# Optimization experiments

Measured on AMD Instinct MI355X. Metric: run time of the kernel, lower is better.

The kernel has to match this reference:

```python
import jax, jax.numpy as jnp
import numpy as np

EPS_RMS = 1e-6
EPS_Q = 1e-5
EPS_NORM = 1e-10


def _rmsnorm(x):
    return x * jax.lax.rsqrt(jnp.mean(x * x, axis=-1, keepdims=True) + EPS_RMS)


def _activation_quant(x):
    # per-token 8-bit absmax quantization (BitNet b1.58)
    scale = 127.0 / jnp.maximum(jnp.max(jnp.abs(x), axis=-1, keepdims=True), EPS_Q)
    return jnp.clip(jnp.round(x * scale), -128.0, 127.0) / scale


def _weight_quant(w):
    # per-tensor ternary quantization with mean-abs scale
    scale = 1.0 / jnp.maximum(jnp.mean(jnp.abs(w)), EPS_Q)
    return jnp.clip(jnp.round(w * scale), -1.0, 1.0) / scale


def _bitlinear(x, w, b):
    xn = _rmsnorm(x)
    xq = xn + jax.lax.stop_gradient(_activation_quant(xn) - xn)  # STE
    wq = w + jax.lax.stop_gradient(_weight_quant(w) - w)         # STE
    return jnp.einsum('bsf,of->bso', xq, wq) + b


def setup_inputs() -> dict:
    key = jax.random.key(0)
    ks = jax.random.split(key, 4)
    B, S, F = 32, 1024, 512
    evidence_features = jax.random.normal(ks[0], (B, S, F), dtype=jnp.float32)
    prior_belief = jax.random.uniform(ks[1], (B, S, F), dtype=jnp.float32)
    W1 = jax.random.normal(ks[2], (F, 2 * F), dtype=jnp.float32) * (1.0 / np.sqrt(2 * F))
    b1 = jnp.zeros((F,), dtype=jnp.float32)
    W2 = jax.random.normal(ks[3], (F, F), dtype=jnp.float32) * (1.0 / np.sqrt(F))
    b2 = jnp.zeros((F,), dtype=jnp.float32)
    return {"evidence_features": evidence_features, "prior_belief": prior_belief,
            "W1": W1, "b1": b1, "W2": W2, "b2": b2}


def reference(evidence_features, prior_belief, W1, b1, W2, b2):
    # belief_update MLP on concat(prior, evidence)
    update_input = jnp.concatenate([prior_belief, evidence_features], axis=-1)  # [B,S,2F]
    h = jax.nn.relu(_bitlinear(update_input, W1, b1))                           # [B,S,F]
    likelihood_factors = jax.nn.sigmoid(_bitlinear(h, W2, b2))                  # [B,S,F]
    posterior_unnorm = prior_belief * likelihood_factors
    normalizer = jnp.maximum(jnp.sum(posterior_unnorm, axis=1, keepdims=True), EPS_NORM)
    return posterior_unnorm / normalizer
```

## Files before the change

kernel.cpp:

```cpp
#include <hip/hip_runtime.h>
#include <math.h>

typedef __attribute__((ext_vector_type(4))) int i32x4;
typedef __attribute__((ext_vector_type(4))) float f32x4;

#define GLOAD_LDS16(g, l)                                          \
  __builtin_amdgcn_global_load_lds(                                \
      (const __attribute__((address_space(1))) void*)(g),          \
      (__attribute__((address_space(3))) void*)(l), 16, 0, 0)

__global__ void kWabs(const float* __restrict__ w1, const float* __restrict__ w2,
                      double* __restrict__ part) {
  const bool second = blockIdx.x >= 256;
  const float* w = second ? w2 : w1;
  const int n = second ? 262144 : 524288;
  int t = (blockIdx.x & 255) * 256 + threadIdx.x;
  double s = 0.0;
  for (int i = t; i < n; i += 65536) s += (double)fabsf(w[i]);
#pragma unroll
  for (int m = 32; m >= 1; m >>= 1) s += __shfl_xor(s, m);
  __shared__ double sd[4];
  int lane = threadIdx.x & 63, wid = threadIdx.x >> 6;
  if (lane == 0) sd[wid] = s;
  __syncthreads();
  if (threadIdx.x == 0) part[blockIdx.x] = (sd[0] + sd[1]) + (sd[2] + sd[3]);
}

__global__ void kWfin(const double* __restrict__ part, float* __restrict__ wsv) {
  const double* p = part + blockIdx.x * 256;
  const double n = (blockIdx.x == 0) ? 524288.0 : 262144.0;
  double s = p[threadIdx.x];
#pragma unroll
  for (int m = 32; m >= 1; m >>= 1) s += __shfl_xor(s, m);
  __shared__ double sd[4];
  int lane = threadIdx.x & 63, wid = threadIdx.x >> 6;
  if (lane == 0) sd[wid] = s;
  __syncthreads();
  if (threadIdx.x == 0) {
    double tot = (sd[0] + sd[1]) + (sd[2] + sd[3]);
    wsv[blockIdx.x] = fmaxf((float)(tot / n), 1e-5f);
  }
}

__global__ void kWq(const float* __restrict__ w1, const float* __restrict__ w2,
                    const float* __restrict__ wsv,
                    char* __restrict__ wq1, char* __restrict__ wq2) {
  const bool second = blockIdx.x >= 2048;
  const float* w = second ? w2 : w1;
  char* wq = second ? wq2 : wq1;
  const float scale = 1.0f / wsv[second ? 1 : 0];
  int i = (second ? blockIdx.x - 2048 : blockIdx.x) * 256 + threadIdx.x;
  float q = fminf(fmaxf(rintf(w[i] * scale), -1.0f), 1.0f);
  wq[i] = (char)(int)q;
}

__global__ __launch_bounds__(512, 4) void kFused1(
    const float* __restrict__ prior, const float* __restrict__ evid,
    const char* __restrict__ Wq, const float* __restrict__ biasG,
    const float* __restrict__ wS,
    char* __restrict__ XqOut, float* __restrict__ rActOut) {
  __shared__ __align__(16) union {
    char Ap[65536];
    struct { float sq[64][8]; float mx[64][8]; } ep;
  } u;
  __shared__ float rowSc[64];
  __shared__ float biasS[512];

  const int tid = threadIdx.x;
  const int lane = tid & 63;
  const int wn = tid >> 6;
  const int lr = lane & 15;
  const int kg = lane >> 4;
  const size_t row0 = (size_t)blockIdx.x * 64;

  biasS[tid] = biasG[tid];

  {
    const int lc = lane * 4;
    const float* pp = prior + (row0 + wn * 8) * 512 + lc;
    const float* pe = evid + (row0 + wn * 8) * 512 + lc;
    f32x4 x0 = *(const f32x4*)pp;
    f32x4 x1 = *(const f32x4*)(pp + 256);
    f32x4 x2 = *(const f32x4*)pe;
    f32x4 x3 = *(const f32x4*)(pe + 256);
#pragma unroll
    for (int rr = 0; rr < 8; ++rr) {
      f32x4 y0, y1, y2, y3;
      if (rr < 7) {
        const float* np = pp + (rr + 1) * 512;
        const float* ne = pe + (rr + 1) * 512;
        y0 = *(const f32x4*)np; y1 = *(const f32x4*)(np + 256);
        y2 = *(const f32x4*)ne; y3 = *(const f32x4*)(ne + 256);
      }
      float ss = 0.f, mx = 0.f;
      f32x4 xs[4] = {x0, x1, x2, x3};
#pragma unroll
      for (int v = 0; v < 4; ++v)
#pragma unroll
        for (int i = 0; i < 4; ++i) { float f = xs[v][i]; ss += f * f; mx = fmaxf(mx, fabsf(f)); }
#pragma unroll
      for (int m = 32; m >= 1; m >>= 1) { ss += __shfl_xor(ss, m); mx = fmaxf(mx, __shfl_xor(mx, m)); }
      const float inv = 1.0f / sqrtf(ss * (1.0f / 1024.0f) + 1e-6f);
      const float amax = fmaxf(mx * inv, 1e-5f);
      const float s = 127.0f / amax;
      int pk[4];
#pragma unroll
      for (int v = 0; v < 4; ++v) {
        int p = 0;
#pragma unroll
        for (int i = 0; i < 4; ++i) {
          int qi = (int)fminf(fmaxf(rintf(xs[v][i] * inv * s), -128.0f), 127.0f);
          p |= (qi & 255) << (8 * i);
        }
        pk[v] = p;
      }
      const int r = wn * 8 + rr;
      const int base = r * 1024 + (lc ^ ((r & 7) << 4));
      *(int*)&u.Ap[base] = pk[0];
      *(int*)&u.Ap[base + 256] = pk[1];
      *(int*)&u.Ap[base + 512] = pk[2];
      *(int*)&u.Ap[base + 768] = pk[3];
      if (lane == 0) rowSc[r] = amax / 127.0f;
      if (rr < 7) { x0 = y0; x1 = y1; x2 = y2; x3 = y3; }
    }
  }

  i32x4 acc[4][4];
#pragma unroll
  for (int a = 0; a < 4; ++a)
#pragma unroll
    for (int b = 0; b < 4; ++b) acc[a][b] = (i32x4){0, 0, 0, 0};

  const char* gBl = Wq + (size_t)(wn * 64 + lr) * 1024 + kg * 16;
  i32x4 bf[4];
#pragma unroll
  for (int fn = 0; fn < 4; ++fn)
    bf[fn] = *(const i32x4*)(gBl + fn * 16384);

  __syncthreads();

  const int aswz = (lr & 7) << 4;
#pragma unroll 2
  for (int kt = 0; kt < 16; ++kt) {
    i32x4 bn[4];
    if (kt < 15) {
#pragma unroll
      for (int fn = 0; fn < 4; ++fn)
        bn[fn] = *(const i32x4*)(gBl + (kt + 1) * 64 + fn * 16384);
    }
    const int acol = (kt * 64 + kg * 16) ^ aswz;
    i32x4 af[4];
#pragma unroll
    for (int fm = 0; fm < 4; ++fm)
      af[fm] = *(const i32x4*)&u.Ap[(fm * 16 + lr) * 1024 + acol];
#pragma unroll
    for (int fn = 0; fn < 4; ++fn)
#pragma unroll
      for (int fm = 0; fm < 4; ++fm)
        acc[fm][fn] = __builtin_amdgcn_mfma_i32_16x16x64_i8(af[fm], bf[fn], acc[fm][fn], 0, 0, 0);
#pragma unroll
    for (int fn = 0; fn < 4; ++fn) bf[fn] = bn[fn];
  }

  __syncthreads();

  const float wsv_ = wS[0];
  f32x4 fa[4][4];
#pragma unroll
  for (int fm = 0; fm < 4; ++fm) {
    float sc[4];
#pragma unroll
    for (int j = 0; j < 4; ++j) sc[j] = rowSc[fm * 16 + kg * 4 + j] * wsv_;
#pragma unroll
    for (int fn = 0; fn < 4; ++fn) {
      const float bb = biasS[wn * 64 + fn * 16 + lr];
#pragma unroll
      for (int j = 0; j < 4; ++j)
        fa[fm][fn][j] = fmaxf((float)acc[fm][fn][j] * sc[j] + bb, 0.0f);
    }
  }
#pragma unroll
  for (int fm = 0; fm < 4; ++fm)
#pragma unroll
    for (int j = 0; j < 4; ++j) {
      float ss = 0.f, mx = 0.f;
#pragma unroll
      for (int fn = 0; fn < 4; ++fn) { float h = fa[fm][fn][j]; ss += h * h; mx = fmaxf(mx, h); }
#pragma unroll
      for (int m = 8; m >= 1; m >>= 1) { ss += __shfl_xor(ss, m); mx = fmaxf(mx, __shfl_xor(mx, m)); }
      if (lr == 0) {
        int rl = fm * 16 + kg * 4 + j;
        u.ep.sq[rl][wn] = ss;
        u.ep.mx[rl][wn] = mx;
      }
    }
  __syncthreads();
#pragma unroll
  for (int fm = 0; fm < 4; ++fm)
#pragma unroll
    for (int j = 0; j < 4; ++j) {
      const int rl = fm * 16 + kg * 4 + j;
      float sst = 0.f, mxt = 0.f;
#pragma unroll
      for (int w = 0; w < 8; ++w) {
        sst += u.ep.sq[rl][w];
        mxt = fmaxf(mxt, u.ep.mx[rl][w]);
      }
      float inv = 1.0f / sqrtf(sst * (1.0f / 512.0f) + 1e-6f);
      float amax = fmaxf(mxt * inv, 1e-5f);
      float s = 127.0f / amax;
      if (lr == 0 && wn == 0) rActOut[row0 + rl] = amax / 127.0f;
#pragma unroll
      for (int fn = 0; fn < 4; ++fn) {
        float xn = fa[fm][fn][j] * inv;
        int qi = (int)fminf(fmaxf(rintf(xn * s), -128.0f), 127.0f);
        XqOut[(row0 + rl) * 512 + wn * 64 + fn * 16 + lr] = (char)qi;
      }
    }
}

__global__ __launch_bounds__(512, 4) void kGemm2(
    const char* __restrict__ Xq, const char* __restrict__ Wq,
    const float* __restrict__ biasG, const float* __restrict__ rAct,
    const float* __restrict__ wS, const float* __restrict__ prior,
    float* __restrict__ outUn, float* __restrict__ partG) {
  __shared__ __align__(16) char A[32768];
  __shared__ float rowR[64];
  __shared__ float biasS[512];
  __shared__ float normPart[512];

  const int tid = threadIdx.x;
  const int lane = tid & 63;
  const int wn = tid >> 6;
  const int lr = lane & 15;
  const int kg = lane >> 4;
  const size_t row0 = (size_t)blockIdx.x * 64;

  if (tid < 64) rowR[tid] = rAct[row0 + tid];
  biasS[tid] = biasG[tid];

#pragma unroll
  for (int i = 0; i < 4; ++i) {
    const int r = i * 16 + wn * 2 + (lane >> 5);
    const int cs = ((lane & 31) * 16) ^ ((r & 7) << 4);
    GLOAD_LDS16(Xq + (row0 + r) * 512 + cs, &A[i * 8192 + wn * 1024]);
  }

  const char* gBl = Wq + (size_t)(wn * 64 + lr) * 512 + kg * 16;
  i32x4 bf[4];
#pragma unroll
  for (int fn = 0; fn < 4; ++fn)
    bf[fn] = *(const i32x4*)(gBl + fn * 8192);

  i32x4 acc[4][4];
#pragma unroll
  for (int a = 0; a < 4; ++a)
#pragma unroll
    for (int b = 0; b < 4; ++b) acc[a][b] = (i32x4){0, 0, 0, 0};

  __syncthreads();

  const int aswz = (lr & 7) << 4;
#pragma unroll 2
  for (int kt = 0; kt < 8; ++kt) {
    i32x4 bn[4];
    if (kt < 7) {
#pragma unroll
      for (int fn = 0; fn < 4; ++fn)
        bn[fn] = *(const i32x4*)(gBl + (kt + 1) * 64 + fn * 8192);
    }
    const int acol = (kt * 64 + kg * 16) ^ aswz;
    i32x4 af[4];
#pragma unroll
    for (int fm = 0; fm < 4; ++fm)
      af[fm] = *(const i32x4*)&A[(fm * 16 + lr) * 512 + acol];
#pragma unroll
    for (int fn = 0; fn < 4; ++fn)
#pragma unroll
      for (int fm = 0; fm < 4; ++fm)
        acc[fm][fn] = __builtin_amdgcn_mfma_i32_16x16x64_i8(af[fm], bf[fn], acc[fm][fn], 0, 0, 0);
#pragma unroll
    for (int fn = 0; fn < 4; ++fn) bf[fn] = bn[fn];
  }

  const float wsv_ = wS[0];
  float colsum[4] = {0.f, 0.f, 0.f, 0.f};
#pragma unroll
  for (int fm = 0; fm < 4; ++fm) {
    float sc[4];
#pragma unroll
    for (int j = 0; j < 4; ++j) sc[j] = rowR[fm * 16 + kg * 4 + j] * wsv_;
#pragma unroll
    for (int fn = 0; fn < 4; ++fn) {
      const int col = wn * 64 + fn * 16 + lr;
      const float bb = biasS[col];
#pragma unroll
      for (int j = 0; j < 4; ++j) {
        const size_t rg = row0 + fm * 16 + kg * 4 + j;
        float v = (float)acc[fm][fn][j] * sc[j] + bb;
        float like = 1.0f / (1.0f + expf(-v));
        float un = prior[rg * 512 + col] * like;
        outUn[rg * 512 + col] = un;
        colsum[fn] += un;
      }
    }
  }
#pragma unroll
  for (int fn = 0; fn < 4; ++fn) {
    colsum[fn] += __shfl_xor(colsum[fn], 16);
    colsum[fn] += __shfl_xor(colsum[fn], 32);
  }
  if (lane < 16) {
#pragma unroll
    for (int fn = 0; fn < 4; ++fn) normPart[wn * 64 + fn * 16 + lane] = colsum[fn];
  }
  __syncthreads();
  partG[(size_t)blockIdx.x * 512 + tid] = normPart[tid];
}

__global__ void kNorm1(const float* __restrict__ partG, float* __restrict__ normA) {
  const int b = blockIdx.x, f = threadIdx.x;
  float s = 0.f;
#pragma unroll
  for (int i = 0; i < 16; ++i) s += partG[(size_t)(b * 16 + i) * 512 + f];
  normA[b * 512 + f] = fmaxf(s, 1e-10f);
}

__global__ void kNorm2(float* __restrict__ out, const float* __restrict__ normA) {
  const size_t i4 = (size_t)blockIdx.x * blockDim.x + threadIdx.x;
  f32x4 v = ((const f32x4*)out)[i4];
  const int f4 = (int)(i4 & 127);
  const int b = (int)(i4 >> 17);
  f32x4 n = ((const f32x4*)normA)[b * 128 + f4];
  v[0] /= n[0]; v[1] /= n[1]; v[2] /= n[2]; v[3] /= n[3];
  ((f32x4*)out)[i4] = v;
}

extern "C" void kernel_launch(void* const* d_in, const int* in_sizes, int n_in,
                              void* d_out, int out_size, void* d_ws, size_t ws_size,
                              hipStream_t stream) {
  const float* evid  = (const float*)d_in[0];
  const float* prior = (const float*)d_in[1];
  const float* W1    = (const float*)d_in[2];
  const float* b1    = (const float*)d_in[3];
  const float* W2    = (const float*)d_in[4];
  const float* b2    = (const float*)d_in[5];
  float* out = (float*)d_out;

  char* ws = (char*)d_ws;
  char*   X2q   = ws;
  char*   W1q   = ws + 16777216;
  char*   W2q   = ws + 17301504;
  float*  r2    = (float*)(ws + 17563648);
  double* part  = (double*)(ws + 17694720);
  float*  wsv   = (float*)(ws + 17698816);
  float*  partG = (float*)(ws + 17699072);
  float*  normA = (float*)(ws + 18747648);

  kWabs<<<512, 256, 0, stream>>>(W1, W2, part);
  kWfin<<<2, 256, 0, stream>>>(part, wsv);
  kWq<<<3072, 256, 0, stream>>>(W1, W2, wsv, W1q, W2q);
  kFused1<<<512, 512, 0, stream>>>(prior, evid, W1q, b1, wsv + 0, X2q, r2);
  kGemm2<<<512, 512, 0, stream>>>(X2q, W2q, b2, r2, wsv + 1, prior, out, partG);
  kNorm1<<<32, 512, 0, stream>>>(partG, normA);
  kNorm2<<<16384, 256, 0, stream>>>(out, normA);
}
```

Baseline: 135.6 us.

## Recompute GEMM2 twice to fuse normalization and drop unnormalized output round-trip

Removes the kNorm1/kNorm2 kernels. GEMM2 now runs twice: the first pass only produces per-block column sums, and the second pass reduces those partials itself and writes the normalized output directly. This avoids writing the 64MB unnormalized tensor and then reading and writing it again, at the cost of repeating the int8 GEMM, sigmoid and prior read. It also double-buffers B-fragment prefetch two steps ahead with full unroll in both GEMMs, and processes rows in pairs during kFused1's quantization prologue to gain more memory-level parallelism.

```diff
diff --git a/kernel.cpp b/kernel.cpp
--- a/kernel.cpp
+++ b/kernel.cpp
@@ -79,49 +79,71 @@
     const int lc = lane * 4;
     const float* pp = prior + (row0 + wn * 8) * 512 + lc;
     const float* pe = evid + (row0 + wn * 8) * 512 + lc;
-    f32x4 x0 = *(const f32x4*)pp;
-    f32x4 x1 = *(const f32x4*)(pp + 256);
-    f32x4 x2 = *(const f32x4*)pe;
-    f32x4 x3 = *(const f32x4*)(pe + 256);
-#pragma unroll
-    for (int rr = 0; rr < 8; ++rr) {
-      f32x4 y0, y1, y2, y3;
-      if (rr < 7) {
-        const float* np = pp + (rr + 1) * 512;
-        const float* ne = pe + (rr + 1) * 512;
-        y0 = *(const f32x4*)np; y1 = *(const f32x4*)(np + 256);
-        y2 = *(const f32x4*)ne; y3 = *(const f32x4*)(ne + 256);
-      }
-      float ss = 0.f, mx = 0.f;
-      f32x4 xs[4] = {x0, x1, x2, x3};
-#pragma unroll
-      for (int v = 0; v < 4; ++v)
-#pragma unroll
-        for (int i = 0; i < 4; ++i) { float f = xs[v][i]; ss += f * f; mx = fmaxf(mx, fabsf(f)); }
-#pragma unroll
-      for (int m = 32; m >= 1; m >>= 1) { ss += __shfl_xor(ss, m); mx = fmaxf(mx, __shfl_xor(mx, m)); }
-      const float inv = 1.0f / sqrtf(ss * (1.0f / 1024.0f) + 1e-6f);
-      const float amax = fmaxf(mx * inv, 1e-5f);
-      const float s = 127.0f / amax;
-      int pk[4];
-#pragma unroll
-      for (int v = 0; v < 4; ++v) {
-        int p = 0;
-#pragma unroll
-        for (int i = 0; i < 4; ++i) {
-          int qi = (int)fminf(fmaxf(rintf(xs[v][i] * inv * s), -128.0f), 127.0f);
-          p |= (qi & 255) << (8 * i);
+    f32x4 x[2][4];
+#pragma unroll
+    for (int r = 0; r < 2; ++r) {
+      x[r][0] = *(const f32x4*)(pp + r * 512);
+      x[r][1] = *(const f32x4*)(pp + r * 512 + 256);
+      x[r][2] = *(const f32x4*)(pe + r * 512);
+      x[r][3] = *(const f32x4*)(pe + r * 512 + 256);
+    }
+#pragma unroll
+    for (int pr = 0; pr < 4; ++pr) {
+      f32x4 y[2][4];
+      if (pr < 3) {
+#pragma unroll
+        for (int r = 0; r < 2; ++r) {
+          const float* np = pp + (pr * 2 + 2 + r) * 512;
+          const float* ne = pe + (pr * 2 + 2 + r) * 512;
+          y[r][0] = *(const f32x4*)np; y[r][1] = *(const f32x4*)(np + 256);
+          y[r][2] = *(const f32x4*)ne; y[r][3] = *(const f32x4*)(ne + 256);
         }
-        pk[v] = p;
-      }
-      const int r = wn * 8 + rr;
-      const int base = r * 1024 + (lc ^ ((r & 7) << 4));
-      *(int*)&u.Ap[base] = pk[0];
-      *(int*)&u.Ap[base + 256] = pk[1];
-      *(int*)&u.Ap[base + 512] = pk[2];
-      *(int*)&u.Ap[base + 768] = pk[3];
-      if (lane == 0) rowSc[r] = amax / 127.0f;
-      if (rr < 7) { x0 = y0; x1 = y1; x2 = y2; x3 = y3; }
+      }
+      float ss[2] = {0.f, 0.f}, mx[2] = {0.f, 0.f};
+#pragma unroll
+      for (int r = 0; r < 2; ++r)
+#pragma unroll
+        for (int v = 0; v < 4; ++v)
+#pragma unroll
+          for (int i = 0; i < 4; ++i) {
+            float f = x[r][v][i];
+            ss[r] += f * f; mx[r] = fmaxf(mx[r], fabsf(f));
+          }
+#pragma unroll
+      for (int m = 32; m >= 1; m >>= 1) {
+        ss[0] += __shfl_xor(ss[0], m); ss[1] += __shfl_xor(ss[1], m);
+        mx[0] = fmaxf(mx[0], __shfl_xor(mx[0], m)); mx[1] = fmaxf(mx[1], __shfl_xor(mx[1], m));
+      }
+#pragma unroll
+      for (int r = 0; r < 2; ++r) {
+        const float inv = 1.0f / sqrtf(ss[r] * (1.0f / 1024.0f) + 1e-6f);
+        const float amax = fmaxf(mx[r] * inv, 1e-5f);
+        const float s = 127.0f / amax;
+        int pk[4];
+#pragma unroll
+        for (int v = 0; v < 4; ++v) {
+          int p = 0;
+#pragma unroll
+          for (int i = 0; i < 4; ++i) {
+            int qi = (int)fminf(fmaxf(rintf(x[r][v][i] * inv * s), -128.0f), 127.0f);
+            p |= (qi & 255) << (8 * i);
+          }
+          pk[v] = p;
+        }
+        const int rw = wn * 8 + pr * 2 + r;
+        const int base = rw * 1024 + (lc ^ ((rw & 7) << 4));
+        *(int*)&u.Ap[base] = pk[0];
+        *(int*)&u.Ap[base + 256] = pk[1];
+        *(int*)&u.Ap[base + 512] = pk[2];
+        *(int*)&u.Ap[base + 768] = pk[3];
+        if (lane == 0) rowSc[rw] = amax / 127.0f;
+      }
+      if (pr < 3) {
+#pragma unroll
+        for (int r = 0; r < 2; ++r)
+#pragma unroll
+          for (int v = 0; v < 4; ++v) x[r][v] = y[r][v];
+      }
     }
   }
 
@@ -132,22 +154,19 @@
     for (int b = 0; b < 4; ++b) acc[a][b] = (i32x4){0, 0, 0, 0};
 
   const char* gBl = Wq + (size_t)(wn * 64 + lr) * 1024 + kg * 16;
-  i32x4 bf[4];
-#pragma unroll
-  for (int fn = 0; fn < 4; ++fn)
-    bf[fn] = *(const i32x4*)(gBl + fn * 16384);
+  i32x4 bf0[4], bf1[4];
+#pragma unroll
+  for (int fn = 0; fn < 4; ++fn) {
+    bf0[fn] = *(const i32x4*)(gBl + fn * 16384);
+    bf1[fn] = *(const i32x4*)(gBl + 64 + fn * 16384);
+  }
 
   __syncthreads();
 
   const int aswz = (lr & 7) << 4;
-#pragma unroll 2
+#pragma unroll
   for (int kt = 0; kt < 16; ++kt) {
-    i32x4 bn[4];
-    if (kt < 15) {
-#pragma unroll
-      for (int fn = 0; fn < 4; ++fn)
-        bn[fn] = *(const i32x4*)(gBl + (kt + 1) * 64 + fn * 16384);
-    }
+    i32x4(&bfc)[4] = (kt & 1) ? bf1 : bf0;
     const int acol = (kt * 64 + kg * 16) ^ aswz;
     i32x4 af[4];
 #pragma unroll
@@ -157,9 +176,12 @@
     for (int fn = 0; fn < 4; ++fn)
 #pragma unroll
       for (int fm = 0; fm < 4; ++fm)
-        acc[fm][fn] = __builtin_amdgcn_mfma_i32_16x16x64_i8(af[fm], bf[fn], acc[fm][fn], 0, 0, 0);
-#pragma unroll
-    for (int fn = 0; fn < 4; ++fn) bf[fn] = bn[fn];
+        acc[fm][fn] = __builtin_amdgcn_mfma_i32_16x16x64_i8(af[fm], bfc[fn], acc[fm][fn], 0, 0, 0);
+    if (kt + 2 < 16) {
+#pragma unroll
+      for (int fn = 0; fn < 4; ++fn)
+        bfc[fn] = *(const i32x4*)(gBl + (kt + 2) * 64 + fn * 16384);
+    }
   }
 
   __syncthreads();
@@ -219,15 +241,16 @@
     }
 }
 
+template <bool WRITE_PASS>
 __global__ __launch_bounds__(512, 4) void kGemm2(
     const char* __restrict__ Xq, const char* __restrict__ Wq,
     const float* __restrict__ biasG, const float* __restrict__ rAct,
     const float* __restrict__ wS, const float* __restrict__ prior,
-    float* __restrict__ outUn, float* __restrict__ partG) {
+    float* __restrict__ outp, float* __restrict__ partG) {
   __shared__ __align__(16) char A[32768];
   __shared__ float rowR[64];
   __shared__ float biasS[512];
-  __shared__ float normPart[512];
+  __shared__ float normS[512];
 
   const int tid = threadIdx.x;
   const int lane = tid & 63;
@@ -246,11 +269,21 @@
     GLOAD_LDS16(Xq + (row0 + r) * 512 + cs, &A[i * 8192 + wn * 1024]);
   }
 
+  if constexpr (WRITE_PASS) {
+    const int b = blockIdx.x >> 4;
+    float ns = 0.f;
+#pragma unroll
+    for (int i = 0; i < 16; ++i) ns += partG[(size_t)(b * 16 + i) * 512 + tid];
+    normS[tid] = fmaxf(ns, 1e-10f);
+  }
+
   const char* gBl = Wq + (size_t)(wn * 64 + lr) * 512 + kg * 16;
-  i32x4 bf[4];
-#pragma unroll
-  for (int fn = 0; fn < 4; ++fn)
-    bf[fn] = *(const i32x4*)(gBl + fn * 8192);
+  i32x4 bf0[4], bf1[4];
+#pragma unroll
+  for (int fn = 0; fn < 4; ++fn) {
+    bf0[fn] = *(const i32x4*)(gBl + fn * 8192);
+    bf1[fn] = *(const i32x4*)(gBl + 64 + fn * 8192);
+  }
 
   i32x4 acc[4][4];
 #pragma unroll
@@ -261,14 +294,9 @@
   __syncthreads();
 
   const int aswz = (lr & 7) << 4;
-#pragma unroll 2
+#pragma unroll
   for (int kt = 0; kt < 8; ++kt) {
-    i32x4 bn[4];
-    if (kt < 7) {
-#pragma unroll
-      for (int fn = 0; fn < 4; ++fn)
-        bn[fn] = *(const i32x4*)(gBl + (kt + 1) * 64 + fn * 8192);
-    }
+    i32x4(&bfc)[4] = (kt & 1) ? bf1 : bf0;
     const int acol = (kt * 64 + kg * 16) ^ aswz;
     i32x4 af[4];
 #pragma unroll
@@ -278,62 +306,69 @@
     for (int fn = 0; fn < 4; ++fn)
 #pragma unroll
       for (int fm = 0; fm < 4; ++fm)
-        acc[fm][fn] = __builtin_amdgcn_mfma_i32_16x16x64_i8(af[fm], bf[fn], acc[fm][fn], 0, 0, 0);
-#pragma unroll
-    for (int fn = 0; fn < 4; ++fn) bf[fn] = bn[fn];
+        acc[fm][fn] = __builtin_amdgcn_mfma_i32_16x16x64_i8(af[fm], bfc[fn], acc[fm][fn], 0, 0, 0);
+    if (kt + 2 < 8) {
+#pragma unroll
+      for (int fn = 0; fn < 4; ++fn)
+        bfc[fn] = *(const i32x4*)(gBl + (kt + 2) * 64 + fn * 8192);
+    }
   }
 
   const float wsv_ = wS[0];
-  float colsum[4] = {0.f, 0.f, 0.f, 0.f};
-#pragma unroll
-  for (int fm = 0; fm < 4; ++fm) {
-    float sc[4];
-#pragma unroll
-    for (int j = 0; j < 4; ++j) sc[j] = rowR[fm * 16 + kg * 4 + j] * wsv_;
+  if constexpr (!WRITE_PASS) {
+    float colsum[4] = {0.f, 0.f, 0.f, 0.f};
+#pragma unroll
+    for (int fm = 0; fm < 4; ++fm) {
+      float sc[4];
+#pragma unroll
+      for (int j = 0; j < 4; ++j) sc[j] = rowR[fm * 16 + kg * 4 + j] * wsv_;
+#pragma unroll
+      for (int fn = 0; fn < 4; ++fn) {
+        const int col = wn * 64 + fn * 16 + lr;
+        const float bb = biasS[col];
+#pragma unroll
+        for (int j = 0; j < 4; ++j) {
+          const size_t rg = row0 + fm * 16 + kg * 4 + j;
+          float v = (float)acc[fm][fn][j] * sc[j] + bb;
+          float like = 1.0f / (1.0f + expf(-v));
+          float un = prior[rg * 512 + col] * like;
+          colsum[fn] += un;
+        }
+      }
+    }
 #pragma unroll
     for (int fn = 0; fn < 4; ++fn) {
-      const int col = wn * 64 + fn * 16 + lr;
-      const float bb = biasS[col];
-#pragma unroll
-      for (int j = 0; j < 4; ++j) {
-        const size_t rg = row0 + fm * 16 + kg * 4 + j;
-        float v = (float)acc[fm][fn][j] * sc[j] + bb;
-        float like = 1.0f / (1.0f + expf(-v));
-        float un = prior[rg * 512 + col] * like;
-        outUn[rg * 512 + col] = un;
-        colsum[fn] += un;
-      }
-    }
-  }
-#pragma unroll
-  for (int fn = 0; fn < 4; ++fn) {
-    colsum[fn] += __shfl_xor(colsum[fn], 16);
-    colsum[fn] += __shfl_xor(colsum[fn], 32);
-  }
-  if (lane < 16) {
-#pragma unroll
-    for (int fn = 0; fn < 4; ++fn) normPart[wn * 64 + fn * 16 + lane] = colsum[fn];
-  }
-  __syncthreads();
-  partG[(size_t)blockIdx.x * 512 + tid] = normPart[tid];
-}
-
-__global__ void kNorm1(const float* __restrict__ partG, float* __restrict__ normA) {
-  const int b = blockIdx.x, f = threadIdx.x;
-  float s = 0.f;
-#pragma unroll
-  for (int i = 0; i < 16; ++i) s += partG[(size_t)(b * 16 + i) * 512 + f];
-  normA[b * 512 + f] = fmaxf(s, 1e-10f);
-}
-
-__global__ void kNorm2(float* __restrict__ out, const float* __restrict__ normA) {
-  const size_t i4 = (size_t)blockIdx.x * blockDim.x + threadIdx.x;
-  f32x4 v = ((const f32x4*)out)[i4];
-  const int f4 = (int)(i4 & 127);
-  const int b = (int)(i4 >> 17);
-  f32x4 n = ((const f32x4*)normA)[b * 128 + f4];
-  v[0] /= n[0]; v[1] /= n[1]; v[2] /= n[2]; v[3] /= n[3];
-  ((f32x4*)out)[i4] = v;
+      colsum[fn] += __shfl_xor(colsum[fn], 16);
+      colsum[fn] += __shfl_xor(colsum[fn], 32);
+    }
+    if (lane < 16) {
+#pragma unroll
+      for (int fn = 0; fn < 4; ++fn) normS[wn * 64 + fn * 16 + lane] = colsum[fn];
+    }
+    __syncthreads();
+    partG[(size_t)blockIdx.x * 512 + tid] = normS[tid];
+  } else {
+#pragma unroll
+    for (int fm = 0; fm < 4; ++fm) {
+      float sc[4];
+#pragma unroll
+      for (int j = 0; j < 4; ++j) sc[j] = rowR[fm * 16 + kg * 4 + j] * wsv_;
+#pragma unroll
+      for (int fn = 0; fn < 4; ++fn) {
+        const int col = wn * 64 + fn * 16 + lr;
+        const float bb = biasS[col];
+        const float nrm = normS[col];
+#pragma unroll
+        for (int j = 0; j < 4; ++j) {
+          const size_t rg = row0 + fm * 16 + kg * 4 + j;
+          float v = (float)acc[fm][fn][j] * sc[j] + bb;
+          float like = 1.0f / (1.0f + expf(-v));
+          float un = prior[rg * 512 + col] * like;
+          outp[rg * 512 + col] = un / nrm;
+        }
+      }
+    }
+  }
 }
 
 extern "C" void kernel_launch(void* const* d_in, const int* in_sizes, int n_in,
@@ -355,13 +390,11 @@
   double* part  = (double*)(ws + 17694720);
   float*  wsv   = (float*)(ws + 17698816);
   float*  partG = (float*)(ws + 17699072);
-  float*  normA = (float*)(ws + 18747648);
 
   kWabs<<<512, 256, 0, stream>>>(W1, W2, part);
   kWfin<<<2, 256, 0, stream>>>(part, wsv);
   kWq<<<3072, 256, 0, stream>>>(W1, W2, wsv, W1q, W2q);
   kFused1<<<512, 512, 0, stream>>>(prior, evid, W1q, b1, wsv + 0, X2q, r2);
-  kGemm2<<<512, 512, 0, stream>>>(X2q, W2q, b2, r2, wsv + 1, prior, out, partG);
-  kNorm1<<<32, 512, 0, stream>>>(partG, normA);
-  kNorm2<<<16384, 256, 0, stream>>>(out, normA);
-}
+  kGemm2<false><<<512, 512, 0, stream>>>(X2q, W2q, b2, r2, wsv + 1, prior, nullptr, partG);
+  kGemm2<true><<<512, 512, 0, stream>>>(X2q, W2q, b2, r2, wsv + 1, prior, out, partG);
+}
```

New measurement: 154.4 us. +13.9%, slower.
